# Kernel tuning notes

Hardware: AMD Instinct MI355X
Metric: run time of the kernel (lower is better)

The kernel has to match this reference:

```python
import jax, jax.numpy as jnp
import numpy as np

B, T, C, H = 8, 2048, 1024, 128

def setup_inputs() -> dict:
    key = jax.random.key(0)
    kx, kq, kk, kv = jax.random.split(key, 4)
    x = jax.random.normal(kx, (B, T, C), dtype=jnp.float32)
    Wq = jax.random.normal(kq, (C, H), dtype=jnp.float32) * 0.02
    Wk = jax.random.normal(kk, (C, H), dtype=jnp.float32) * 0.02
    Wv = jax.random.normal(kv, (C, H), dtype=jnp.float32) * 0.02
    return {"x": x, "Wq": Wq, "Wk": Wk, "Wv": Wv}

def reference(x, Wq, Wk, Wv):
    # q,k,v: [B,T,H] via bias-free dense projections
    q = jnp.einsum('btc,ch->bth', x, Wq)
    k = jnp.einsum('btc,ch->bth', x, Wk)
    v = jnp.einsum('btc,ch->bth', x, Wv)
    scale = k.shape[-1] ** (-0.5)
    # scores: [B,T,T]
    wei = jnp.einsum('bth,bsh->bts', q, k) * scale
    Tlen = x.shape[1]
    causal = jnp.tril(jnp.ones((Tlen, Tlen), dtype=bool))  # True = keep
    wei = jnp.where(causal[None, :, :], wei, -jnp.inf)
    wei = jax.nn.softmax(wei, axis=-1)
    return jnp.einsum('bts,bsh->bth', wei, v)
```

## Files before the change

kernel.cpp:

```cpp
#include <hip/hip_runtime.h>

#define B_ 8
#define T_ 2048
#define C_ 1024
#define H_ 128
#define BT_ (B_*T_)

typedef unsigned short u16;
typedef unsigned int u32;
typedef __attribute__((ext_vector_type(4))) float f32x4;
typedef __attribute__((ext_vector_type(8))) __bf16 bf16x8;

__device__ __forceinline__ u16 f2bf(float f) {
  u32 u = __float_as_uint(f);
  u += 0x7fffu + ((u >> 16) & 1u);
  return (u16)(u >> 16);
}

__device__ __forceinline__ bf16x8 load_frag(const u16* base, int stride, int row0, int k0, int lane) {
  const u16* p = base + (size_t)(row0 + (lane & 15)) * stride + k0 + ((lane >> 4) << 3);
  return *reinterpret_cast<const bf16x8*>(p);
}

__global__ void wt_kernel(const float* __restrict__ Wq, const float* __restrict__ Wk,
                          const float* __restrict__ Wv, u16* __restrict__ wt) {
  int mat = blockIdx.y;
  const float* W = (mat == 0) ? Wq : (mat == 1) ? Wk : Wv;
  int i = blockIdx.x * 256 + threadIdx.x;
  int h = i >> 10;
  int c = i & 1023;
  wt[mat * (C_ * H_) + i] = f2bf(W[c * H_ + h]);
}

__global__ __launch_bounds__(256) void qkv_gemm(const float* __restrict__ x, const u16* __restrict__ wt,
                                                u16* __restrict__ q, u16* __restrict__ k2,
                                                u16* __restrict__ vt) {
  __shared__ __align__(16) u16 As[2][64 * 40];
  __shared__ __align__(16) u16 Bs[2][128 * 40];
  int t = threadIdx.x;
  int lane = t & 63, w = t >> 6;
  int wm = w >> 1, wn = w & 1;
  int quad = lane >> 4, col = lane & 15;
  int m0 = blockIdx.x * 64;
  int mat = blockIdx.y;
  const u16* wmp = wt + mat * (C_ * H_);

  int ar = t >> 2, ac = (t & 3) * 8;
  int br = t >> 2, bc = (t & 3) * 8;

  {
    const float* ap = x + (size_t)(m0 + ar) * C_ + ac;
    float4 a4 = *reinterpret_cast<const float4*>(ap);
    float4 a5 = *reinterpret_cast<const float4*>(ap + 4);
    union { u16 h[8]; uint4 v; } ah;
    ah.h[0] = f2bf(a4.x); ah.h[1] = f2bf(a4.y); ah.h[2] = f2bf(a4.z); ah.h[3] = f2bf(a4.w);
    ah.h[4] = f2bf(a5.x); ah.h[5] = f2bf(a5.y); ah.h[6] = f2bf(a5.z); ah.h[7] = f2bf(a5.w);
    *reinterpret_cast<uint4*>(&As[0][ar * 40 + ac]) = ah.v;
#pragma unroll
    for (int p = 0; p < 2; p++)
      *reinterpret_cast<uint4*>(&Bs[0][(br + 64 * p) * 40 + bc]) =
          *reinterpret_cast<const uint4*>(wmp + (size_t)(br + 64 * p) * C_ + bc);
  }

  f32x4 acc[2][4] = {};
  for (int kk = 0; kk < 32; kk++) {
    int cur = kk & 1;
    __syncthreads();
    bool more = (kk + 1 < 32);
    float4 a4, a5; uint4 b4[2];
    if (more) {
      int kn = (kk + 1) * 32;
      const float* ap = x + (size_t)(m0 + ar) * C_ + kn + ac;
      a4 = *reinterpret_cast<const float4*>(ap);
      a5 = *reinterpret_cast<const float4*>(ap + 4);
#pragma unroll
      for (int p = 0; p < 2; p++)
        b4[p] = *reinterpret_cast<const uint4*>(wmp + (size_t)(br + 64 * p) * C_ + kn + bc);
    }
    const u16* A = &As[cur][0];
    const u16* Bb = &Bs[cur][0];
    bf16x8 af[2], bfr[4];
#pragma unroll
    for (int mt = 0; mt < 2; mt++)
      af[mt] = *reinterpret_cast<const bf16x8*>(&A[(wm * 32 + mt * 16 + col) * 40 + quad * 8]);
#pragma unroll
    for (int nt = 0; nt < 4; nt++)
      bfr[nt] = *reinterpret_cast<const bf16x8*>(&Bb[(wn * 64 + nt * 16 + col) * 40 + quad * 8]);
#pragma unroll
    for (int mt = 0; mt < 2; mt++)
#pragma unroll
      for (int nt = 0; nt < 4; nt++)
        acc[mt][nt] = __builtin_amdgcn_mfma_f32_16x16x32_bf16(af[mt], bfr[nt], acc[mt][nt], 0, 0, 0);
    if (more) {
      int nxt = cur ^ 1;
      union { u16 h[8]; uint4 v; } ah;
      ah.h[0] = f2bf(a4.x); ah.h[1] = f2bf(a4.y); ah.h[2] = f2bf(a4.z); ah.h[3] = f2bf(a4.w);
      ah.h[4] = f2bf(a5.x); ah.h[5] = f2bf(a5.y); ah.h[6] = f2bf(a5.z); ah.h[7] = f2bf(a5.w);
      *reinterpret_cast<uint4*>(&As[nxt][ar * 40 + ac]) = ah.v;
#pragma unroll
      for (int p = 0; p < 2; p++)
        *reinterpret_cast<uint4*>(&Bs[nxt][(br + 64 * p) * 40 + bc]) = b4[p];
    }
  }

#pragma unroll
  for (int mt = 0; mt < 2; mt++) {
#pragma unroll
    for (int nt = 0; nt < 4; nt++) {
#pragma unroll
      for (int r = 0; r < 4; r++) {
        int row = m0 + wm * 32 + mt * 16 + quad * 4 + r;
        int n = wn * 64 + nt * 16 + col;
        u16 val = f2bf(acc[mt][nt][r]);
        if (mat == 0) {
          q[(size_t)row * H_ + n] = val;
        } else if (mat == 1) {
          k2[(size_t)row * H_ + n] = val;
        } else {
          int bb = row >> 11;
          int tt = row & 2047;
          vt[((size_t)bb * H_ + n) * T_ + tt] = val;
        }
      }
    }
  }
}

__global__ __launch_bounds__(256) void attn_part(const u16* __restrict__ q, const u16* __restrict__ k,
                                                 const u16* __restrict__ vt,
                                                 float* __restrict__ Op, float* __restrict__ lsum) {
  __shared__ __align__(16) u16 Ks[2][32 * 136];
  __shared__ __align__(16) u16 Vs[2][128 * 40];
  __shared__ __align__(16) u16 P[4][2][16 * 40];
  int t = threadIdx.x;
  int lane = t & 63, w = t >> 6;
  int quad = lane >> 4, col = lane & 15;
  int bx = blockIdx.x;
  int qt = 31 - (bx >> 4);
  int s = (bx >> 3) & 1;
  int b = bx & 7;
  const float scale = 0.08838834764831845f;

  int nk = 2 * (qt + 1);
  int n0 = qt + 1;
  int it0 = s ? n0 : 0;
  int it1 = s ? nk : n0;

  int krow0 = t >> 4, ke = (t & 15) * 8;
  int krow1 = krow0 + 16;
  int vrow0 = t >> 2, ve = (t & 3) * 8;
  int vrow1 = vrow0 + 64;

  int qrow0 = b * T_ + qt * 64 + w * 16;
  bf16x8 qf[4];
#pragma unroll
  for (int ks = 0; ks < 4; ks++) qf[ks] = load_frag(q, H_, qrow0, ks * 32, lane);

  f32x4 o[8] = {};
  float l[4] = {0.f, 0.f, 0.f, 0.f};
  int myqrow = qt * 64 + w * 16 + quad * 4;

  {
    const u16* kb = k + (size_t)(b * T_ + it0 * 32) * H_;
    *reinterpret_cast<uint4*>(&Ks[0][krow0 * 136 + ke]) = *reinterpret_cast<const uint4*>(kb + (size_t)krow0 * 128 + ke);
    *reinterpret_cast<uint4*>(&Ks[0][krow1 * 136 + ke]) = *reinterpret_cast<const uint4*>(kb + (size_t)krow1 * 128 + ke);
    const u16* vb = vt + (size_t)b * H_ * T_ + it0 * 32;
    *reinterpret_cast<uint4*>(&Vs[0][vrow0 * 40 + ve]) = *reinterpret_cast<const uint4*>(vb + (size_t)vrow0 * T_ + ve);
    *reinterpret_cast<uint4*>(&Vs[0][vrow1 * 40 + ve]) = *reinterpret_cast<const uint4*>(vb + (size_t)vrow1 * T_ + ve);
  }

  for (int kt = it0; kt < it1; kt++) {
    int cur = (kt - it0) & 1;
    __syncthreads();
    bool more = (kt + 1 < it1);
    uint4 kc0, kc1, vc0, vc1;
    if (more) {
      const u16* kb = k + (size_t)(b * T_ + (kt + 1) * 32) * H_;
      kc0 = *reinterpret_cast<const uint4*>(kb + (size_t)krow0 * 128 + ke);
      kc1 = *reinterpret_cast<const uint4*>(kb + (size_t)krow1 * 128 + ke);
      const u16* vb = vt + (size_t)b * H_ * T_ + (kt + 1) * 32;
      vc0 = *reinterpret_cast<const uint4*>(vb + (size_t)vrow0 * T_ + ve);
      vc1 = *reinterpret_cast<const uint4*>(vb + (size_t)vrow1 * T_ + ve);
    }

    f32x4 s0 = {}, s1 = {};
#pragma unroll
    for (int ks = 0; ks < 4; ks++) {
      bf16x8 kb0 = *reinterpret_cast<const bf16x8*>(&Ks[cur][col * 136 + ks * 32 + quad * 8]);
      bf16x8 kb1 = *reinterpret_cast<const bf16x8*>(&Ks[cur][(col + 16) * 136 + ks * 32 + quad * 8]);
      s0 = __builtin_amdgcn_mfma_f32_16x16x32_bf16(qf[ks], kb0, s0, 0, 0, 0);
      s1 = __builtin_amdgcn_mfma_f32_16x16x32_bf16(qf[ks], kb1, s1, 0, 0, 0);
    }

    float pv[8];
    int kcol0 = kt * 32 + col;
#pragma unroll
    for (int r = 0; r < 4; r++) {
      int qr = myqrow + r;
      float a0 = fminf(s0[r] * scale, 30.f);
      float a1 = fminf(s1[r] * scale, 30.f);
      a0 = (kcol0      > qr) ? -1e30f : a0;
      a1 = (kcol0 + 16 > qr) ? -1e30f : a1;
      float p0 = __expf(a0);
      float p1 = __expf(a1);
      pv[r] = p0; pv[4 + r] = p1;
      l[r] += p0 + p1;
    }

    u16* Pb = &P[w][cur][0];
#pragma unroll
    for (int r = 0; r < 4; r++) {
      Pb[(quad * 4 + r) * 40 + col] = f2bf(pv[r]);
      Pb[(quad * 4 + r) * 40 + col + 16] = f2bf(pv[4 + r]);
    }
    asm volatile("" ::: "memory");
    __builtin_amdgcn_s_waitcnt(0xc07f);
    asm volatile("" ::: "memory");
    bf16x8 pf = *reinterpret_cast<const bf16x8*>(&Pb[col * 40 + (quad << 3)]);

#pragma unroll
    for (int ht = 0; ht < 8; ht++) {
      bf16x8 vf = *reinterpret_cast<const bf16x8*>(&Vs[cur][(ht * 16 + col) * 40 + quad * 8]);
      o[ht] = __builtin_amdgcn_mfma_f32_16x16x32_bf16(pf, vf, o[ht], 0, 0, 0);
    }

    if (more) {
      int nxt = cur ^ 1;
      *reinterpret_cast<uint4*>(&Ks[nxt][krow0 * 136 + ke]) = kc0;
      *reinterpret_cast<uint4*>(&Ks[nxt][krow1 * 136 + ke]) = kc1;
      *reinterpret_cast<uint4*>(&Vs[nxt][vrow0 * 40 + ve]) = vc0;
      *reinterpret_cast<uint4*>(&Vs[nxt][vrow1 * 40 + ve]) = vc1;
    }
  }

#pragma unroll
  for (int r = 0; r < 4; r++) {
    float v = l[r];
    v += __shfl_xor(v, 1);
    v += __shfl_xor(v, 2);
    v += __shfl_xor(v, 4);
    v += __shfl_xor(v, 8);
    l[r] = v;
  }

  int tile = (s * 8 + b) * 32 + qt;
  float* Orow = Op + (size_t)tile * (64 * 128);
  float* lrow = lsum + (size_t)tile * 64;
  int rowin0 = w * 16 + quad * 4;
  if (col == 0) {
#pragma unroll
    for (int r = 0; r < 4; r++) lrow[rowin0 + r] = l[r];
  }
#pragma unroll
  for (int ht = 0; ht < 8; ht++) {
#pragma unroll
    for (int r = 0; r < 4; r++)
      Orow[(size_t)(rowin0 + r) * 128 + ht * 16 + col] = o[ht][r];
  }
}

__global__ __launch_bounds__(256) void attn_comb(const float* __restrict__ Op, const float* __restrict__ lsum,
                                                 float* __restrict__ out) {
  int bx = blockIdx.x;
  int b = bx >> 5, qt = bx & 31;
  int t = threadIdx.x;
  int h = t & 127, half = t >> 7;
  int tile0 = b * 32 + qt;
  int tile1 = tile0 + 256;
#pragma unroll 4
  for (int rr = 0; rr < 32; rr++) {
    int row = half * 32 + rr;
    float l0 = lsum[tile0 * 64 + row];
    float l1 = lsum[tile1 * 64 + row];
    float rl = 1.f / (l0 + l1);
    float v = (Op[(size_t)tile0 * 8192 + row * 128 + h] +
               Op[(size_t)tile1 * 8192 + row * 128 + h]) * rl;
    out[((size_t)(b * T_ + qt * 64 + row)) * H_ + h] = v;
  }
}

extern "C" void kernel_launch(void* const* d_in, const int* in_sizes, int n_in,
                              void* d_out, int out_size, void* d_ws, size_t ws_size,
                              hipStream_t stream) {
  (void)in_sizes; (void)n_in; (void)out_size; (void)ws_size;
  const float* x  = (const float*)d_in[0];
  const float* Wq = (const float*)d_in[1];
  const float* Wk = (const float*)d_in[2];
  const float* Wv = (const float*)d_in[3];
  u16* ws = (u16*)d_ws;
  u16* q  = ws;
  u16* k  = ws + (size_t)BT_ * H_;
  u16* vt = ws + 2 * (size_t)BT_ * H_;
  u16* wt = ws + 3 * (size_t)BT_ * H_;
  float* Op = (float*)(ws + 3 * (size_t)BT_ * H_ + 3 * C_ * H_);
  float* lsum = Op + (size_t)512 * 64 * 128;
  float* out = (float*)d_out;

  wt_kernel<<<dim3(512, 3), 256, 0, stream>>>(Wq, Wk, Wv, wt);
  qkv_gemm<<<dim3(BT_ / 64, 3), 256, 0, stream>>>(x, wt, q, k, vt);
  attn_part<<<dim3(512), 256, 0, stream>>>(q, k, vt, Op, lsum);
  attn_comb<<<dim3(256), 256, 0, stream>>>(Op, lsum, out);
}
```

Before: 170.8 us.

## Pre-convert x to bf16 and load GEMM/attention tiles with direct global-to-LDS DMA

Adds a prep kernel that converts x to bf16 once, writing it into workspace, and merges the weight transpose into the same launch. The QKV GEMM now uses 128-row tiles and fills LDS with global_load_lds DMA into XOR-swizzled layouts instead of staging through registers. The attention kernel's K and V tiles are loaded the same way with swizzled offsets. The aim is to cut register staging, the repeated fp32-to-bf16 conversion per N-tile, and LDS bank conflicts, at the cost of an extra full pass over x and reuse of the xb buffer for Op.

```diff
diff --git a/kernel.cpp b/kernel.cpp
--- a/kernel.cpp
+++ b/kernel.cpp
@@ -17,99 +17,118 @@
   return (u16)(u >> 16);
 }
 
+__device__ __forceinline__ void dma16(const u16* g, u16* l) {
+  __builtin_amdgcn_global_load_lds(
+      (const __attribute__((address_space(1))) u32*)g,
+      (__attribute__((address_space(3))) u32*)l, 16, 0, 0);
+}
+
 __device__ __forceinline__ bf16x8 load_frag(const u16* base, int stride, int row0, int k0, int lane) {
   const u16* p = base + (size_t)(row0 + (lane & 15)) * stride + k0 + ((lane >> 4) << 3);
   return *reinterpret_cast<const bf16x8*>(p);
 }
 
-__global__ void wt_kernel(const float* __restrict__ Wq, const float* __restrict__ Wk,
-                          const float* __restrict__ Wv, u16* __restrict__ wt) {
-  int mat = blockIdx.y;
-  const float* W = (mat == 0) ? Wq : (mat == 1) ? Wk : Wv;
-  int i = blockIdx.x * 256 + threadIdx.x;
-  int h = i >> 10;
-  int c = i & 1023;
-  wt[mat * (C_ * H_) + i] = f2bf(W[c * H_ + h]);
-}
-
-__global__ __launch_bounds__(256) void qkv_gemm(const float* __restrict__ x, const u16* __restrict__ wt,
+__global__ __launch_bounds__(256) void prep_kernel(const float* __restrict__ x,
+                                                   const float* __restrict__ Wq,
+                                                   const float* __restrict__ Wk,
+                                                   const float* __restrict__ Wv,
+                                                   u16* __restrict__ xb, u16* __restrict__ wt) {
+  int blk = blockIdx.x, t = threadIdx.x;
+  if (blk < 2048) {
+    size_t base = (size_t)blk * 8192 + t * 8;
+#pragma unroll
+    for (int j = 0; j < 4; j++) {
+      size_t i = base + (size_t)j * 2048;
+      float4 a = *reinterpret_cast<const float4*>(x + i);
+      float4 b = *reinterpret_cast<const float4*>(x + i + 4);
+      union { u16 h[8]; uint4 v; } r;
+      r.h[0] = f2bf(a.x); r.h[1] = f2bf(a.y); r.h[2] = f2bf(a.z); r.h[3] = f2bf(a.w);
+      r.h[4] = f2bf(b.x); r.h[5] = f2bf(b.y); r.h[6] = f2bf(b.z); r.h[7] = f2bf(b.w);
+      *reinterpret_cast<uint4*>(xb + i) = r.v;
+    }
+  } else {
+    int tid = (blk - 2048) * 256 + t;
+#pragma unroll 4
+    for (int rep = 0; rep < 192; rep++) {
+      int g = rep * 2048 + tid;
+      int mat = g >> 17;
+      int i = g & 131071;
+      int h = i >> 10, c = i & 1023;
+      const float* W = (mat == 0) ? Wq : (mat == 1) ? Wk : Wv;
+      wt[g] = f2bf(W[c * H_ + h]);
+    }
+  }
+}
+
+__global__ __launch_bounds__(256) void qkv_gemm(const u16* __restrict__ xb, const u16* __restrict__ wt,
                                                 u16* __restrict__ q, u16* __restrict__ k2,
                                                 u16* __restrict__ vt) {
-  __shared__ __align__(16) u16 As[2][64 * 40];
-  __shared__ __align__(16) u16 Bs[2][128 * 40];
+  __shared__ __align__(16) u16 As[2][4096];
+  __shared__ __align__(16) u16 Bs[2][4096];
   int t = threadIdx.x;
   int lane = t & 63, w = t >> 6;
   int wm = w >> 1, wn = w & 1;
   int quad = lane >> 4, col = lane & 15;
-  int m0 = blockIdx.x * 64;
+  int m0 = blockIdx.x * 128;
   int mat = blockIdx.y;
-  const u16* wmp = wt + mat * (C_ * H_);
-
-  int ar = t >> 2, ac = (t & 3) * 8;
-  int br = t >> 2, bc = (t & 3) * 8;
-
-  {
-    const float* ap = x + (size_t)(m0 + ar) * C_ + ac;
-    float4 a4 = *reinterpret_cast<const float4*>(ap);
-    float4 a5 = *reinterpret_cast<const float4*>(ap + 4);
-    union { u16 h[8]; uint4 v; } ah;
-    ah.h[0] = f2bf(a4.x); ah.h[1] = f2bf(a4.y); ah.h[2] = f2bf(a4.z); ah.h[3] = f2bf(a4.w);
-    ah.h[4] = f2bf(a5.x); ah.h[5] = f2bf(a5.y); ah.h[6] = f2bf(a5.z); ah.h[7] = f2bf(a5.w);
-    *reinterpret_cast<uint4*>(&As[0][ar * 40 + ac]) = ah.v;
-#pragma unroll
-    for (int p = 0; p < 2; p++)
-      *reinterpret_cast<uint4*>(&Bs[0][(br + 64 * p) * 40 + bc]) =
-          *reinterpret_cast<const uint4*>(wmp + (size_t)(br + 64 * p) * C_ + bc);
-  }
-
-  f32x4 acc[2][4] = {};
+  const u16* wtm = wt + mat * (C_ * H_);
+
+  int rj[2], oj[2];
+#pragma unroll
+  for (int j = 0; j < 2; j++) {
+    int c = (j * 4 + w) * 64 + lane;
+    int r = c >> 2;
+    int qg = (c & 3) ^ ((r >> 1) & 3);
+    rj[j] = r; oj[j] = qg * 8;
+  }
+
+#pragma unroll
+  for (int j = 0; j < 2; j++) {
+    dma16(xb + (size_t)(m0 + rj[j]) * C_ + oj[j], &As[0][(j * 4 + w) * 512]);
+    dma16(wtm + (size_t)rj[j] * C_ + oj[j], &Bs[0][(j * 4 + w) * 512]);
+  }
+
+  int aoff[4], boff[4];
+#pragma unroll
+  for (int mt = 0; mt < 4; mt++) {
+    int row = wm * 64 + mt * 16 + col;
+    aoff[mt] = (4 * row + (quad ^ ((row >> 1) & 3))) * 8;
+    int rowb = wn * 64 + mt * 16 + col;
+    boff[mt] = (4 * rowb + (quad ^ ((rowb >> 1) & 3))) * 8;
+  }
+
+  f32x4 acc[4][4] = {};
   for (int kk = 0; kk < 32; kk++) {
     int cur = kk & 1;
     __syncthreads();
-    bool more = (kk + 1 < 32);
-    float4 a4, a5; uint4 b4[2];
-    if (more) {
+    if (kk + 1 < 32) {
+      int nxt = cur ^ 1;
       int kn = (kk + 1) * 32;
-      const float* ap = x + (size_t)(m0 + ar) * C_ + kn + ac;
-      a4 = *reinterpret_cast<const float4*>(ap);
-      a5 = *reinterpret_cast<const float4*>(ap + 4);
-#pragma unroll
-      for (int p = 0; p < 2; p++)
-        b4[p] = *reinterpret_cast<const uint4*>(wmp + (size_t)(br + 64 * p) * C_ + kn + bc);
-    }
-    const u16* A = &As[cur][0];
-    const u16* Bb = &Bs[cur][0];
-    bf16x8 af[2], bfr[4];
-#pragma unroll
-    for (int mt = 0; mt < 2; mt++)
-      af[mt] = *reinterpret_cast<const bf16x8*>(&A[(wm * 32 + mt * 16 + col) * 40 + quad * 8]);
-#pragma unroll
-    for (int nt = 0; nt < 4; nt++)
-      bfr[nt] = *reinterpret_cast<const bf16x8*>(&Bb[(wn * 64 + nt * 16 + col) * 40 + quad * 8]);
-#pragma unroll
-    for (int mt = 0; mt < 2; mt++)
+#pragma unroll
+      for (int j = 0; j < 2; j++) {
+        dma16(xb + (size_t)(m0 + rj[j]) * C_ + kn + oj[j], &As[nxt][(j * 4 + w) * 512]);
+        dma16(wtm + (size_t)rj[j] * C_ + kn + oj[j], &Bs[nxt][(j * 4 + w) * 512]);
+      }
+    }
+    bf16x8 af[4], bfr[4];
+#pragma unroll
+    for (int mt = 0; mt < 4; mt++) af[mt] = *reinterpret_cast<const bf16x8*>(&As[cur][aoff[mt]]);
+#pragma unroll
+    for (int nt = 0; nt < 4; nt++) bfr[nt] = *reinterpret_cast<const bf16x8*>(&Bs[cur][boff[nt]]);
+#pragma unroll
+    for (int mt = 0; mt < 4; mt++)
 #pragma unroll
       for (int nt = 0; nt < 4; nt++)
         acc[mt][nt] = __builtin_amdgcn_mfma_f32_16x16x32_bf16(af[mt], bfr[nt], acc[mt][nt], 0, 0, 0);
-    if (more) {
-      int nxt = cur ^ 1;
-      union { u16 h[8]; uint4 v; } ah;
-      ah.h[0] = f2bf(a4.x); ah.h[1] = f2bf(a4.y); ah.h[2] = f2bf(a4.z); ah.h[3] = f2bf(a4.w);
-      ah.h[4] = f2bf(a5.x); ah.h[5] = f2bf(a5.y); ah.h[6] = f2bf(a5.z); ah.h[7] = f2bf(a5.w);
-      *reinterpret_cast<uint4*>(&As[nxt][ar * 40 + ac]) = ah.v;
-#pragma unroll
-      for (int p = 0; p < 2; p++)
-        *reinterpret_cast<uint4*>(&Bs[nxt][(br + 64 * p) * 40 + bc]) = b4[p];
-    }
-  }
-
-#pragma unroll
-  for (int mt = 0; mt < 2; mt++) {
+  }
+
+#pragma unroll
+  for (int mt = 0; mt < 4; mt++) {
 #pragma unroll
     for (int nt = 0; nt < 4; nt++) {
 #pragma unroll
       for (int r = 0; r < 4; r++) {
-        int row = m0 + wm * 32 + mt * 16 + quad * 4 + r;
+        int row = m0 + wm * 64 + mt * 16 + quad * 4 + r;
         int n = wn * 64 + nt * 16 + col;
         u16 val = f2bf(acc[mt][nt][r]);
         if (mat == 0) {
@@ -129,8 +148,8 @@
 __global__ __launch_bounds__(256) void attn_part(const u16* __restrict__ q, const u16* __restrict__ k,
                                                  const u16* __restrict__ vt,
                                                  float* __restrict__ Op, float* __restrict__ lsum) {
-  __shared__ __align__(16) u16 Ks[2][32 * 136];
-  __shared__ __align__(16) u16 Vs[2][128 * 40];
+  __shared__ __align__(16) u16 Ks[2][4096];
+  __shared__ __align__(16) u16 Vs[2][4096];
   __shared__ __align__(16) u16 P[4][2][16 * 40];
   int t = threadIdx.x;
   int lane = t & 63, w = t >> 6;
@@ -146,15 +165,30 @@
   int it0 = s ? n0 : 0;
   int it1 = s ? nk : n0;
 
-  int krow0 = t >> 4, ke = (t & 15) * 8;
-  int krow1 = krow0 + 16;
-  int vrow0 = t >> 2, ve = (t & 3) * 8;
-  int vrow1 = vrow0 + 64;
+  int krj[2], koj[2], vrj[2], voj[2];
+#pragma unroll
+  for (int j = 0; j < 2; j++) {
+    int c = (j * 4 + w) * 64 + lane;
+    int rk = c >> 4; krj[j] = rk; koj[j] = ((c & 15) ^ (rk & 7)) * 8;
+    int rv = c >> 2; vrj[j] = rv; voj[j] = (((c & 3) ^ ((rv >> 1) & 3))) * 8;
+  }
 
   int qrow0 = b * T_ + qt * 64 + w * 16;
   bf16x8 qf[4];
 #pragma unroll
   for (int ks = 0; ks < 4; ks++) qf[ks] = load_frag(q, H_, qrow0, ks * 32, lane);
+
+  int k0off[4], k1off[4], voff[8];
+#pragma unroll
+  for (int ks = 0; ks < 4; ks++) {
+    k0off[ks] = (16 * col + ((ks * 4 + quad) ^ (col & 7))) * 8;
+    k1off[ks] = (16 * (col + 16) + ((ks * 4 + quad) ^ (col & 7))) * 8;
+  }
+#pragma unroll
+  for (int ht = 0; ht < 8; ht++) {
+    int row = ht * 16 + col;
+    voff[ht] = (4 * row + (quad ^ ((row >> 1) & 3))) * 8;
+  }
 
   f32x4 o[8] = {};
   float l[4] = {0.f, 0.f, 0.f, 0.f};
@@ -162,32 +196,33 @@
 
   {
     const u16* kb = k + (size_t)(b * T_ + it0 * 32) * H_;
-    *reinterpret_cast<uint4*>(&Ks[0][krow0 * 136 + ke]) = *reinterpret_cast<const uint4*>(kb + (size_t)krow0 * 128 + ke);
-    *reinterpret_cast<uint4*>(&Ks[0][krow1 * 136 + ke]) = *reinterpret_cast<const uint4*>(kb + (size_t)krow1 * 128 + ke);
     const u16* vb = vt + (size_t)b * H_ * T_ + it0 * 32;
-    *reinterpret_cast<uint4*>(&Vs[0][vrow0 * 40 + ve]) = *reinterpret_cast<const uint4*>(vb + (size_t)vrow0 * T_ + ve);
-    *reinterpret_cast<uint4*>(&Vs[0][vrow1 * 40 + ve]) = *reinterpret_cast<const uint4*>(vb + (size_t)vrow1 * T_ + ve);
+#pragma unroll
+    for (int j = 0; j < 2; j++) {
+      dma16(kb + (size_t)krj[j] * H_ + koj[j], &Ks[0][(j * 4 + w) * 512]);
+      dma16(vb + (size_t)vrj[j] * T_ + voj[j], &Vs[0][(j * 4 + w) * 512]);
+    }
   }
 
   for (int kt = it0; kt < it1; kt++) {
     int cur = (kt - it0) & 1;
     __syncthreads();
-    bool more = (kt + 1 < it1);
-    uint4 kc0, kc1, vc0, vc1;
-    if (more) {
+    if (kt + 1 < it1) {
+      int nxt = cur ^ 1;
       const u16* kb = k + (size_t)(b * T_ + (kt + 1) * 32) * H_;
-      kc0 = *reinterpret_cast<const uint4*>(kb + (size_t)krow0 * 128 + ke);
-      kc1 = *reinterpret_cast<const uint4*>(kb + (size_t)krow1 * 128 + ke);
       const u16* vb = vt + (size_t)b * H_ * T_ + (kt + 1) * 32;
-      vc0 = *reinterpret_cast<const uint4*>(vb + (size_t)vrow0 * T_ + ve);
-      vc1 = *reinterpret_cast<const uint4*>(vb + (size_t)vrow1 * T_ + ve);
+#pragma unroll
+      for (int j = 0; j < 2; j++) {
+        dma16(kb + (size_t)krj[j] * H_ + koj[j], &Ks[nxt][(j * 4 + w) * 512]);
+        dma16(vb + (size_t)vrj[j] * T_ + voj[j], &Vs[nxt][(j * 4 + w) * 512]);
+      }
     }
 
     f32x4 s0 = {}, s1 = {};
 #pragma unroll
     for (int ks = 0; ks < 4; ks++) {
-      bf16x8 kb0 = *reinterpret_cast<const bf16x8*>(&Ks[cur][col * 136 + ks * 32 + quad * 8]);
-      bf16x8 kb1 = *reinterpret_cast<const bf16x8*>(&Ks[cur][(col + 16) * 136 + ks * 32 + quad * 8]);
+      bf16x8 kb0 = *reinterpret_cast<const bf16x8*>(&Ks[cur][k0off[ks]]);
+      bf16x8 kb1 = *reinterpret_cast<const bf16x8*>(&Ks[cur][k1off[ks]]);
       s0 = __builtin_amdgcn_mfma_f32_16x16x32_bf16(qf[ks], kb0, s0, 0, 0, 0);
       s1 = __builtin_amdgcn_mfma_f32_16x16x32_bf16(qf[ks], kb1, s1, 0, 0, 0);
     }
@@ -220,16 +255,8 @@
 
 #pragma unroll
     for (int ht = 0; ht < 8; ht++) {
-      bf16x8 vf = *reinterpret_cast<const bf16x8*>(&Vs[cur][(ht * 16 + col) * 40 + quad * 8]);
+      bf16x8 vf = *reinterpret_cast<const bf16x8*>(&Vs[cur][voff[ht]]);
       o[ht] = __builtin_amdgcn_mfma_f32_16x16x32_bf16(pf, vf, o[ht], 0, 0, 0);
-    }
-
-    if (more) {
-      int nxt = cur ^ 1;
-      *reinterpret_cast<uint4*>(&Ks[nxt][krow0 * 136 + ke]) = kc0;
-      *reinterpret_cast<uint4*>(&Ks[nxt][krow1 * 136 + ke]) = kc1;
-      *reinterpret_cast<uint4*>(&Vs[nxt][vrow0 * 40 + ve]) = vc0;
-      *reinterpret_cast<uint4*>(&Vs[nxt][vrow1 * 40 + ve]) = vc1;
     }
   }
 
@@ -288,16 +315,17 @@
   const float* Wk = (const float*)d_in[2];
   const float* Wv = (const float*)d_in[3];
   u16* ws = (u16*)d_ws;
-  u16* q  = ws;
-  u16* k  = ws + (size_t)BT_ * H_;
-  u16* vt = ws + 2 * (size_t)BT_ * H_;
-  u16* wt = ws + 3 * (size_t)BT_ * H_;
-  float* Op = (float*)(ws + 3 * (size_t)BT_ * H_ + 3 * C_ * H_);
+  u16* xb = ws;
+  u16* q  = ws + (size_t)BT_ * C_;
+  u16* k  = q + (size_t)BT_ * H_;
+  u16* vt = k + (size_t)BT_ * H_;
+  u16* wt = vt + (size_t)BT_ * H_;
+  float* Op = (float*)xb;
   float* lsum = Op + (size_t)512 * 64 * 128;
   float* out = (float*)d_out;
 
-  wt_kernel<<<dim3(512, 3), 256, 0, stream>>>(Wq, Wk, Wv, wt);
-  qkv_gemm<<<dim3(BT_ / 64, 3), 256, 0, stream>>>(x, wt, q, k, vt);
+  prep_kernel<<<dim3(2056), 256, 0, stream>>>(x, Wq, Wk, Wv, xb, wt);
+  qkv_gemm<<<dim3(128, 3), 256, 0, stream>>>(xb, wt, q, k, vt);
   attn_part<<<dim3(512), 256, 0, stream>>>(q, k, vt, Op, lsum);
   attn_comb<<<dim3(256), 256, 0, stream>>>(Op, lsum, out);
 }
```

Result: slower. 198.1 us (+15.9%).
